# Performance work log

Hardware: AMD Instinct MI355X
Metric: run time of the kernel (lower is better)

The kernel has to match this reference:

```python
import jax, jax.numpy as jnp
import numpy as np
import math

def setup_inputs() -> dict:
    key = jax.random.key(0)
    k1, k2, k3 = jax.random.split(key, 3)
    B, S, E = 2, 2048, 1024
    H, D = 16, 64
    inputs = jax.random.normal(k1, (B, S, E), dtype=jnp.float32)
    Wqkv = jax.random.uniform(k2, (E, 3 * H * D), minval=-0.1, maxval=0.1, dtype=jnp.float32)
    Wo = jax.random.uniform(k3, (H * D, E), minval=-0.1, maxval=0.1, dtype=jnp.float32)
    return {"inputs": inputs, "Wqkv": Wqkv, "Wo": Wo, "nhead": H}

def reference(inputs, Wqkv, Wo, nhead):
    B, S, E = inputs.shape
    H = int(nhead)
    D = Wqkv.shape[1] // (3 * H)
    causal, ghost = True, True

    qkv = jnp.matmul(inputs, Wqkv)                       # (B, S, 3*H*D)
    qkv = qkv.reshape(B, S, 3, H, D)
    Q = qkv[:, :, 0].transpose(0, 2, 1, 3)               # (B, H, S, D)
    K = qkv[:, :, 1].transpose(0, 2, 1, 3)
    V = qkv[:, :, 2].transpose(0, 2, 1, 3)

    scores = jnp.einsum('bhqd,bhkd->bhqk', Q, K) / math.sqrt(D)
    if causal:
        neg_inf = jnp.float32(-jnp.inf)
        mask = jnp.where(jnp.triu(jnp.ones((S, S), dtype=bool), k=1), neg_inf, jnp.float32(0.0))
        scores = scores + mask  # broadcast over (B, H)

    # ghost softmax: standard stable softmax but denominator gets +1
    z = jnp.exp(scores - jnp.max(scores, axis=-1, keepdims=True))
    denom = jnp.sum(z, axis=-1, keepdims=True)
    if ghost:
        denom = denom + jnp.float32(1.0)
    attn = z / denom                                      # (B, H, S, S)

    A = jnp.einsum('bhqk,bhkd->bhqd', attn, V)            # (B, H, S, D)
    A = A.transpose(0, 2, 1, 3).reshape(B, S, H * D)      # (B, S, H*D)
    return jnp.matmul(A, Wo)
```

## Files before the change

kernel.cpp:

```cpp
#include <hip/hip_runtime.h>

typedef float    f32x4  __attribute__((ext_vector_type(4)));
typedef _Float16 half8  __attribute__((ext_vector_type(8)));
typedef _Float16 half4v __attribute__((ext_vector_type(4)));

#define MFMA16(a,b,c) __builtin_amdgcn_mfma_f32_16x16x32_f16(a,b,c,0,0,0)

__device__ __forceinline__ float exp2_fast(float x){
  float y; asm("v_exp_f32 %0, %1" : "=v"(y) : "v"(x)); return y;
}
__device__ __forceinline__ void gload_lds16(const _Float16* g, _Float16* l){
  __builtin_amdgcn_global_load_lds(
      (const __attribute__((address_space(1))) unsigned int*)(g),
      (__attribute__((address_space(3))) unsigned int*)(l),
      16, 0, 0);
}

#define S_LEN 2048
#define E_DIM 1024
#define H_NUM 16
#define D_DIM 64
#define NBH   32
#define M_ROWS 4096
#define N3    3072
#define LOG2E 1.44269504089f

__global__ __launch_bounds__(256) void prep_kernel(
    const float* __restrict__ X, const float* __restrict__ Wqkv,
    const float* __restrict__ Wo,
    _Float16* __restrict__ Xh, _Float16* __restrict__ Wqh,
    _Float16* __restrict__ Woh)
{
  __shared__ float tile[32][33];
  const int blk = blockIdx.x, tid = threadIdx.x;
  if (blk < 4096){
    const int i = blk * 256 + tid;
    const float4 v = reinterpret_cast<const float4*>(X)[i];
    half4v h;
    h[0] = (_Float16)v.x; h[1] = (_Float16)v.y;
    h[2] = (_Float16)v.z; h[3] = (_Float16)v.w;
    *reinterpret_cast<half4v*>(&Xh[(size_t)i*4]) = h;
    return;
  }
  const float* in; _Float16* out; int R, C, bx, by;
  if (blk < 4096 + 3072){
    const int b2 = blk - 4096;
    in = Wqkv; out = Wqh; R = E_DIM; C = N3;
    bx = (b2 % 96) * 32; by = (b2 / 96) * 32;
  } else {
    const int b2 = blk - 7168;
    in = Wo; out = Woh; R = E_DIM; C = E_DIM;
    bx = (b2 % 32) * 32; by = (b2 / 32) * 32;
  }
  const int tx = tid & 31, ty = tid >> 5;
#pragma unroll
  for (int i = ty; i < 32; i += 8)
    tile[i][tx] = in[(size_t)(by + i) * C + bx + tx];
  __syncthreads();
#pragma unroll
  for (int i = ty; i < 32; i += 8)
    out[(size_t)(bx + i) * R + by + tx] = (_Float16)tile[tx][i];
}

template<int EPI>
__global__ __launch_bounds__(256, 3) void gemm97(
    const _Float16* __restrict__ A, const _Float16* __restrict__ B,
    int Kdim, int Ndim, float* __restrict__ Cout,
    _Float16* __restrict__ qh, _Float16* __restrict__ kh, _Float16* __restrict__ vh)
{
  __shared__ __align__(16) _Float16 sA[128][64], sB[128][64];
  const int tid = threadIdx.x;
  const int nx = gridDim.x, nwg = nx * gridDim.y;
  int bidx = blockIdx.x, bidy = blockIdx.y;
  if ((nwg & 7) == 0){
    const int id = bidx + nx * bidy;
    const int nid = (id & 7) * (nwg >> 3) + (id >> 3);
    bidx = nid % nx; bidy = nid / nx;
  }
  const int m0 = bidy * 128, n0 = bidx * 128;
  const int wid = tid >> 6, lane = tid & 63;
  const int wr = (wid >> 1) * 64, wc = (wid & 1) * 64;
  const int lr = lane & 15, lc = lane >> 4;
  const int ldrow = lane >> 3;
  const int ldcol = ((lane & 7) ^ ldrow) * 8;
  const int swz = (lr & 7) << 4;

  f32x4 acc[4][4] = {};
  const int nK = Kdim >> 6;
  for (int ks = 0; ks < nK; ++ks){
    const int k0 = ks << 6;
#pragma unroll
    for (int cc = 0; cc < 4; ++cc){
      const int c = wid * 4 + cc;
      const int row = c * 8 + ldrow;
      gload_lds16(&A[(size_t)(m0 + row) * Kdim + k0 + ldcol], &sA[c*8][0]);
      gload_lds16(&B[(size_t)(n0 + row) * Kdim + k0 + ldcol], &sB[c*8][0]);
    }
    __syncthreads();
    const char* ab = (const char*)&sA[0][0];
    const char* bb = (const char*)&sB[0][0];
#pragma unroll
    for (int kk = 0; kk < 64; kk += 32){
      half8 fa[4], fb[4];
#pragma unroll
      for (int t = 0; t < 4; ++t){
        fa[t] = *reinterpret_cast<const half8*>(
            ab + (wr + t*16 + lr)*128 + ((kk*2 + lc*16) ^ swz));
        fb[t] = *reinterpret_cast<const half8*>(
            bb + (wc + t*16 + lr)*128 + ((kk*2 + lc*16) ^ swz));
      }
#pragma unroll
      for (int mt = 0; mt < 4; ++mt)
#pragma unroll
        for (int nt = 0; nt < 4; ++nt)
          acc[mt][nt] = MFMA16(fa[mt], fb[nt], acc[mt][nt]);
    }
    __syncthreads();
  }
#pragma unroll
  for (int mt = 0; mt < 4; ++mt)
#pragma unroll
    for (int nt = 0; nt < 4; ++nt)
#pragma unroll
      for (int r = 0; r < 4; ++r){
        const int m = m0 + wr + mt*16 + lc*4 + r;
        const int n = n0 + wc + nt*16 + lr;
        float v = acc[mt][nt][r];
        if (EPI == 0){
          Cout[(size_t)m * Ndim + n] = v;
        } else {
          const int t = n >> 10, rem = n & 1023, hh = rem >> 6, d = rem & 63;
          const int b = m >> 11, s = m & 2047;
          const int bh = b * H_NUM + hh;
          if (t == 0) v *= (0.125f * LOG2E);
          size_t o;
          if (t == 2)  o = ((size_t)bh * D_DIM + d) * S_LEN + s;
          else         o = ((size_t)bh * S_LEN + s) * D_DIM + d;
          _Float16* ph = (t == 0) ? qh : (t == 1) ? kh : vh;
          ph[o] = (_Float16)v;
        }
      }
}

__global__ __launch_bounds__(256, 4) void gemm64(
    const _Float16* __restrict__ A, const _Float16* __restrict__ B,
    int Kdim, int Ndim, float* __restrict__ Cout)
{
  __shared__ __align__(16) _Float16 sA[64][64], sB[128][64];
  const int tid = threadIdx.x;
  const int nx = gridDim.x, nwg = nx * gridDim.y;
  int bidx = blockIdx.x, bidy = blockIdx.y;
  if ((nwg & 7) == 0){
    const int id = bidx + nx * bidy;
    const int nid = (id & 7) * (nwg >> 3) + (id >> 3);
    bidx = nid % nx; bidy = nid / nx;
  }
  const int m0 = bidy * 64, n0 = bidx * 128;
  const int wid = tid >> 6, lane = tid & 63;
  const int wr = (wid >> 1) * 32, wc = (wid & 1) * 64;
  const int lr = lane & 15, lc = lane >> 4;
  const int ldrow = lane >> 3;
  const int ldcol = ((lane & 7) ^ ldrow) * 8;
  const int swz = (lr & 7) << 4;

  f32x4 acc[2][4] = {};
  const int nK = Kdim >> 6;
  for (int ks = 0; ks < nK; ++ks){
    const int k0 = ks << 6;
#pragma unroll
    for (int cc = 0; cc < 2; ++cc){
      const int c = wid * 2 + cc;
      const int row = c * 8 + ldrow;
      gload_lds16(&A[(size_t)(m0 + row) * Kdim + k0 + ldcol], &sA[c*8][0]);
    }
#pragma unroll
    for (int cc = 0; cc < 4; ++cc){
      const int c = wid * 4 + cc;
      const int row = c * 8 + ldrow;
      gload_lds16(&B[(size_t)(n0 + row) * Kdim + k0 + ldcol], &sB[c*8][0]);
    }
    __syncthreads();
    const char* ab = (const char*)&sA[0][0];
    const char* bb = (const char*)&sB[0][0];
#pragma unroll
    for (int kk = 0; kk < 64; kk += 32){
      half8 fa[2], fb[4];
#pragma unroll
      for (int t = 0; t < 2; ++t)
        fa[t] = *reinterpret_cast<const half8*>(
            ab + (wr + t*16 + lr)*128 + ((kk*2 + lc*16) ^ swz));
#pragma unroll
      for (int t = 0; t < 4; ++t)
        fb[t] = *reinterpret_cast<const half8*>(
            bb + (wc + t*16 + lr)*128 + ((kk*2 + lc*16) ^ swz));
#pragma unroll
      for (int mt = 0; mt < 2; ++mt)
#pragma unroll
        for (int nt = 0; nt < 4; ++nt)
          acc[mt][nt] = MFMA16(fa[mt], fb[nt], acc[mt][nt]);
    }
    __syncthreads();
  }
#pragma unroll
  for (int mt = 0; mt < 2; ++mt)
#pragma unroll
    for (int nt = 0; nt < 4; ++nt)
#pragma unroll
      for (int r = 0; r < 4; ++r){
        const int m = m0 + wr + mt*16 + lc*4 + r;
        const int n = n0 + wc + nt*16 + lr;
        Cout[(size_t)m * Ndim + n] = acc[mt][nt][r];
      }
}

__global__ __launch_bounds__(256, 6) void attn_partial(
    const _Float16* __restrict__ Qh, const _Float16* __restrict__ Kh,
    const _Float16* __restrict__ Vth,
    _Float16* __restrict__ Opart, float* __restrict__ Spart)
{
  __shared__ __align__(16) _Float16 sK[64][64];
  __shared__ __align__(16) _Float16 sV[64][64];
  __shared__ __align__(16) _Float16 sP[4][16][64];
  const int tid = threadIdx.x, wid = tid >> 6, lane = tid & 63;
  const int id  = blockIdx.x;
  const int xcd = id & 7, seq = id >> 3;
  const int bh  = xcd + 8 * (seq & 3);
  const int rest = seq >> 2;
  const int qt  = 31 - (rest >> 1);
  const int half = rest & 1;
  const int h0 = (qt + 1) >> 1;
  const int t0 = half ? h0 : 0;
  const int t1 = half ? (qt + 1) : h0;
  const int q0 = qt * 64;
  const int lr = lane & 15, lc = lane >> 4;
  const int swz = (lr & 7) << 4;
  const size_t base = (size_t)bh * S_LEN * D_DIM;

  const int pidx = (bh * 32 + qt) * 2 + half;
  _Float16* Op = Opart + (size_t)pidx * 4096;
  float*    Sp = Spart + (size_t)pidx * 192;

  if (t1 <= t0){
#pragma unroll
    for (int dt = 0; dt < 4; ++dt)
#pragma unroll
      for (int r = 0; r < 4; ++r)
        Op[(wid*16 + lc*4 + r)*64 + dt*16 + lr] = (_Float16)0.f;
    if (lane < 16){
      Sp[wid*16 + lr] = -1e30f;
      Sp[64 + wid*16 + lr] = 0.f;
      Sp[128 + wid*16 + lr] = -1e30f;
    }
    return;
  }

  const int lrow = lane >> 3;
  const int cswz = ((lane & 7) ^ lrow) * 8;

  auto stage = [&](int t){
    const int kv0 = t * 64;
#pragma unroll
    for (int cc = 0; cc < 2; ++cc){
      const int ch = wid * 2 + cc;
      const int row = ch * 8 + lrow;
      gload_lds16(&Kh[base + (size_t)(kv0 + row) * D_DIM + cswz], &sK[ch*8][0]);
      gload_lds16(&Vth[base + (size_t)row * S_LEN + kv0 + cswz], &sV[ch*8][0]);
    }
  };

  half8 fq[2];
  {
    const int qrow = q0 + wid*16 + lr;
#pragma unroll
    for (int kc = 0; kc < 2; ++kc)
      fq[kc] = *reinterpret_cast<const half8*>(&Qh[base + (size_t)qrow * 64 + kc*32 + lc*8]);
  }

  f32x4 acc[4] = {};
  float m = -1e30f, l = 0.f, tm = -1e30f;

#pragma unroll 1
  for (int t = t0; t < t1; ++t){
    __syncthreads();
    stage(t);
    __syncthreads();

    const char* kb = (const char*)&sK[0][0];
    f32x4 sc[4];
    __builtin_amdgcn_s_setprio(1);
#pragma unroll
    for (int nt = 0; nt < 4; ++nt){
      f32x4 z = {};
#pragma unroll
      for (int kc = 0; kc < 2; ++kc){
        const half8 fk = *reinterpret_cast<const half8*>(
            kb + (nt*16 + lr)*128 + ((kc*64 + lc*16) ^ swz));
        z = MFMA16(fk, fq[kc], z);
      }
      sc[nt] = z;
    }
    __builtin_amdgcn_s_setprio(0);

    if (t == qt){
#pragma unroll
      for (int nt = 0; nt < 4; ++nt)
#pragma unroll
        for (int r = 0; r < 4; ++r)
          if (nt*16 + lc*4 + r > wid*16 + lr) sc[nt][r] = -1e30f;
    }

    f32x4 a;
#pragma unroll
    for (int j = 0; j < 4; ++j)
      a[j] = fmaxf(fmaxf(sc[0][j], sc[1][j]), fmaxf(sc[2][j], sc[3][j]));
    float mx = fmaxf(fmaxf(a[0], a[1]), fmaxf(a[2], a[3]));
    mx = fmaxf(mx, __shfl_xor(mx, 16));
    mx = fmaxf(mx, __shfl_xor(mx, 32));
    tm = fmaxf(tm, mx);

    if (__any(mx > m + 8.0f)){
      const float mn = fmaxf(m, mx);
      const float s = exp2_fast(m - mn);
      l *= s; m = mn;
      float rs[4];
#pragma unroll
      for (int r = 0; r < 4; ++r)
        rs[r] = __shfl(s, (lc << 4) | (lc*4 + r), 64);
#pragma unroll
      for (int dt = 0; dt < 4; ++dt)
#pragma unroll
        for (int r = 0; r < 4; ++r) acc[dt][r] *= rs[r];
    }

    f32x4 ssum = {};
#pragma unroll
    for (int nt = 0; nt < 4; ++nt){
#pragma unroll
      for (int r = 0; r < 4; ++r) sc[nt][r] = exp2_fast(sc[nt][r] - m);
      ssum += sc[nt];
    }
    float s1 = (ssum[0] + ssum[1]) + (ssum[2] + ssum[3]);
    s1 += __shfl_xor(s1, 16);
    s1 += __shfl_xor(s1, 32);
    l += s1;

    char* pw = (char*)&sP[wid][0][0];
#pragma unroll
    for (int nt = 0; nt < 4; ++nt){
      int2 pk;
      pk.x = __builtin_bit_cast(int, __builtin_amdgcn_cvt_pkrtz(sc[nt][0], sc[nt][1]));
      pk.y = __builtin_bit_cast(int, __builtin_amdgcn_cvt_pkrtz(sc[nt][2], sc[nt][3]));
      *reinterpret_cast<int2*>(pw + lr*128 + ((nt*32 + lc*8) ^ swz)) = pk;
    }

    const half8 pa0 = *reinterpret_cast<const half8*>(pw + lr*128 + ((lc*16) ^ swz));
    const half8 pa1 = *reinterpret_cast<const half8*>(pw + lr*128 + ((64 + lc*16) ^ swz));

    const char* vb = (const char*)&sV[0][0];
    __builtin_amdgcn_s_setprio(1);
#pragma unroll
    for (int dt = 0; dt < 4; ++dt){
#pragma unroll
      for (int kc = 0; kc < 2; ++kc){
        const half8 fv = *reinterpret_cast<const half8*>(
            vb + (dt*16 + lr)*128 + ((kc*64 + lc*16) ^ swz));
        acc[dt] = MFMA16(kc ? pa1 : pa0, fv, acc[dt]);
      }
    }
    __builtin_amdgcn_s_setprio(0);
  }

#pragma unroll
  for (int dt = 0; dt < 4; ++dt)
#pragma unroll
    for (int r = 0; r < 4; ++r)
      Op[(wid*16 + lc*4 + r)*64 + dt*16 + lr] = (_Float16)acc[dt][r];
  if (lane < 16){
    Sp[wid*16 + lr] = m;
    Sp[64 + wid*16 + lr] = l;
    Sp[128 + wid*16 + lr] = tm;
  }
}

__global__ __launch_bounds__(256) void attn_merge(
    const _Float16* __restrict__ Opart, const float* __restrict__ Spart,
    _Float16* __restrict__ Ao)
{
  const int id = blockIdx.x;
  const int bh = id >> 5, qt = id & 31;
  const int tid = threadIdx.x;
  const int row = tid >> 2, seg = tid & 3;
  const int p0 = (bh * 32 + qt) * 2, p1 = p0 + 1;
  const float* S1 = Spart + (size_t)p0 * 192;
  const float* S2 = Spart + (size_t)p1 * 192;
  const float m1 = S1[row], l1 = S1[64 + row], t1 = S1[128 + row];
  const float m2 = S2[row], l2 = S2[64 + row], t2 = S2[128 + row];
  const float M  = fmaxf(m1, m2);
  const float w1 = exp2_fast(m1 - M), w2 = exp2_fast(m2 - M);
  const float den = l1 * w1 + l2 * w2 + exp2_fast(fmaxf(t1, t2) - M);
  const float inv = 1.0f / den;
  const half8* O1 = reinterpret_cast<const half8*>(Opart + (size_t)p0 * 4096 + row * 64 + seg * 16);
  const half8* O2 = reinterpret_cast<const half8*>(Opart + (size_t)p1 * 4096 + row * 64 + seg * 16);
  const int b = bh >> 4, hh = bh & 15;
  const int q = qt * 64 + row;
  _Float16* dst = Ao + ((size_t)(b * S_LEN + q)) * E_DIM + hh * D_DIM + seg * 16;
#pragma unroll
  for (int v = 0; v < 2; ++v){
    const half8 a1 = O1[v], a2 = O2[v];
    half8 o;
#pragma unroll
    for (int j = 0; j < 8; ++j)
      o[j] = (_Float16)(((float)a1[j] * w1 + (float)a2[j] * w2) * inv);
    reinterpret_cast<half8*>(dst)[v] = o;
  }
}

extern "C" void kernel_launch(void* const* d_in, const int* in_sizes, int n_in,
                              void* d_out, int out_size, void* d_ws, size_t ws_size,
                              hipStream_t stream){
  const float* X    = (const float*)d_in[0];
  const float* Wqkv = (const float*)d_in[1];
  const float* Wo   = (const float*)d_in[2];
  float* out = (float*)d_out;

  _Float16* w = (_Float16*)d_ws;
  size_t off = 0;
  auto alloc = [&](size_t n){ _Float16* p = w + off; off += n; return p; };
  const size_t ME   = (size_t)M_ROWS * E_DIM;
  const size_t WQ   = (size_t)N3 * E_DIM;
  const size_t WOsz = (size_t)E_DIM * E_DIM;
  const size_t QK   = (size_t)NBH * S_LEN * D_DIM;
  _Float16 *Xh = alloc(ME);
  _Float16 *Wqh = alloc(WQ);
  _Float16 *Woh = alloc(WOsz);
  _Float16 *Qh = alloc(QK), *Kh = alloc(QK), *Vth = alloc(QK);
  _Float16 *Ahalf = alloc(ME);
  _Float16 *Opart = alloc((size_t)2048 * 4096);
  _Float16 *Sraw  = alloc((size_t)2048 * 192 * 2);
  float* Spart = (float*)Sraw;

  prep_kernel<<<dim3(8192), 256, 0, stream>>>(X, Wqkv, Wo, Xh, Wqh, Woh);

  gemm97<1><<<dim3(N3/128, M_ROWS/128), 256, 0, stream>>>(
      Xh, Wqh, E_DIM, N3, nullptr, Qh, Kh, Vth);

  attn_partial<<<dim3(2048), 256, 0, stream>>>(Qh, Kh, Vth, Opart, Spart);
  attn_merge<<<dim3(1024), 256, 0, stream>>>(Opart, Spart, Ahalf);

  gemm64<<<dim3(E_DIM/128, M_ROWS/64), 256, 0, stream>>>(
      Ahalf, Woh, E_DIM, E_DIM, out);
}
```

Baseline: 111.3 us.

## Fuse attention partial merge into output projection GEMM prologue

Drops the separate attn_merge kernel and the intermediate fp16 attention buffer. The output-projection GEMM now computes the per-row merge weights into a shared-memory table, then builds each A tile by loading both partial outputs, blending them in registers and storing the result to LDS with the same swizzle as before. This removes one launch plus a full write and read of the merged activations. In exchange, each of the 8 column blocks redoes the merge with double partial reads (likely mostly L2 hits), the A tile loses its async global-to-LDS path, and launch bounds fall to 2 waves per EU.

```diff
diff --git a/kernel.cpp b/kernel.cpp
--- a/kernel.cpp
+++ b/kernel.cpp
@@ -142,11 +142,12 @@
       }
 }
 
-__global__ __launch_bounds__(256, 4) void gemm64(
-    const _Float16* __restrict__ A, const _Float16* __restrict__ B,
-    int Kdim, int Ndim, float* __restrict__ Cout)
+__global__ __launch_bounds__(256, 2) void gemm64f(
+    const _Float16* __restrict__ Opart, const float* __restrict__ Spart,
+    const _Float16* __restrict__ B, float* __restrict__ Cout)
 {
   __shared__ __align__(16) _Float16 sA[64][64], sB[128][64];
+  __shared__ float wTab[16][64][2];
   const int tid = threadIdx.x;
   const int nx = gridDim.x, nwg = nx * gridDim.y;
   int bidx = blockIdx.x, bidy = blockIdx.y;
@@ -156,6 +157,8 @@
     bidx = nid % nx; bidy = nid / nx;
   }
   const int m0 = bidy * 64, n0 = bidx * 128;
+  const int b  = m0 >> 11;
+  const int qt = (m0 & 2047) >> 6;
   const int wid = tid >> 6, lane = tid & 63;
   const int wr = (wid >> 1) * 32, wc = (wid & 1) * 64;
   const int lr = lane & 15, lc = lane >> 4;
@@ -163,21 +166,45 @@
   const int ldcol = ((lane & 7) ^ ldrow) * 8;
   const int swz = (lr & 7) << 4;
 
+  for (int j = tid; j < 1024; j += 256){
+    const int hh = j >> 6, row = j & 63;
+    const int pb = ((b * H_NUM + hh) * 32 + qt) * 2;
+    const float* S1 = Spart + (size_t)pb * 192;
+    const float* S2 = S1 + 192;
+    const float m1 = S1[row], l1 = S1[64 + row], t1v = S1[128 + row];
+    const float m2 = S2[row], l2 = S2[64 + row], t2v = S2[128 + row];
+    const float M  = fmaxf(m1, m2);
+    const float w1 = exp2_fast(m1 - M), w2 = exp2_fast(m2 - M);
+    const float den = l1 * w1 + l2 * w2 + exp2_fast(fmaxf(t1v, t2v) - M);
+    const float inv = 1.0f / den;
+    wTab[hh][row][0] = w1 * inv;
+    wTab[hh][row][1] = w2 * inv;
+  }
+  __syncthreads();
+
   f32x4 acc[2][4] = {};
-  const int nK = Kdim >> 6;
-  for (int ks = 0; ks < nK; ++ks){
+  for (int ks = 0; ks < 16; ++ks){
     const int k0 = ks << 6;
+    const int pbase = ((b * H_NUM + ks) * 32 + qt) * 2;
+    const _Float16* O1 = Opart + (size_t)pbase * 4096;
+    const _Float16* O2 = O1 + 4096;
 #pragma unroll
     for (int cc = 0; cc < 2; ++cc){
-      const int c = wid * 2 + cc;
-      const int row = c * 8 + ldrow;
-      gload_lds16(&A[(size_t)(m0 + row) * Kdim + k0 + ldcol], &sA[c*8][0]);
+      const int row = (wid * 2 + cc) * 8 + ldrow;
+      const half8 a1 = *reinterpret_cast<const half8*>(&O1[row * 64 + ldcol]);
+      const half8 a2 = *reinterpret_cast<const half8*>(&O2[row * 64 + ldcol]);
+      const float w1 = wTab[ks][row][0], w2 = wTab[ks][row][1];
+      half8 av;
+#pragma unroll
+      for (int j = 0; j < 8; ++j)
+        av[j] = (_Float16)((float)a1[j] * w1 + (float)a2[j] * w2);
+      *reinterpret_cast<half8*>((char*)&sA[0][0] + row * 128 + (lane & 7) * 16) = av;
     }
 #pragma unroll
     for (int cc = 0; cc < 4; ++cc){
       const int c = wid * 4 + cc;
       const int row = c * 8 + ldrow;
-      gload_lds16(&B[(size_t)(n0 + row) * Kdim + k0 + ldcol], &sB[c*8][0]);
+      gload_lds16(&B[(size_t)(n0 + row) * E_DIM + k0 + ldcol], &sB[c*8][0]);
     }
     __syncthreads();
     const char* ab = (const char*)&sA[0][0];
@@ -209,7 +236,7 @@
       for (int r = 0; r < 4; ++r){
         const int m = m0 + wr + mt*16 + lc*4 + r;
         const int n = n0 + wc + nt*16 + lr;
-        Cout[(size_t)m * Ndim + n] = acc[mt][nt][r];
+        Cout[(size_t)m * E_DIM + n] = acc[mt][nt][r];
       }
 }
 
@@ -382,39 +409,6 @@
   }
 }
 
-__global__ __launch_bounds__(256) void attn_merge(
-    const _Float16* __restrict__ Opart, const float* __restrict__ Spart,
-    _Float16* __restrict__ Ao)
-{
-  const int id = blockIdx.x;
-  const int bh = id >> 5, qt = id & 31;
-  const int tid = threadIdx.x;
-  const int row = tid >> 2, seg = tid & 3;
-  const int p0 = (bh * 32 + qt) * 2, p1 = p0 + 1;
-  const float* S1 = Spart + (size_t)p0 * 192;
-  const float* S2 = Spart + (size_t)p1 * 192;
-  const float m1 = S1[row], l1 = S1[64 + row], t1 = S1[128 + row];
-  const float m2 = S2[row], l2 = S2[64 + row], t2 = S2[128 + row];
-  const float M  = fmaxf(m1, m2);
-  const float w1 = exp2_fast(m1 - M), w2 = exp2_fast(m2 - M);
-  const float den = l1 * w1 + l2 * w2 + exp2_fast(fmaxf(t1, t2) - M);
-  const float inv = 1.0f / den;
-  const half8* O1 = reinterpret_cast<const half8*>(Opart + (size_t)p0 * 4096 + row * 64 + seg * 16);
-  const half8* O2 = reinterpret_cast<const half8*>(Opart + (size_t)p1 * 4096 + row * 64 + seg * 16);
-  const int b = bh >> 4, hh = bh & 15;
-  const int q = qt * 64 + row;
-  _Float16* dst = Ao + ((size_t)(b * S_LEN + q)) * E_DIM + hh * D_DIM + seg * 16;
-#pragma unroll
-  for (int v = 0; v < 2; ++v){
-    const half8 a1 = O1[v], a2 = O2[v];
-    half8 o;
-#pragma unroll
-    for (int j = 0; j < 8; ++j)
-      o[j] = (_Float16)(((float)a1[j] * w1 + (float)a2[j] * w2) * inv);
-    reinterpret_cast<half8*>(dst)[v] = o;
-  }
-}
-
 extern "C" void kernel_launch(void* const* d_in, const int* in_sizes, int n_in,
                               void* d_out, int out_size, void* d_ws, size_t ws_size,
                               hipStream_t stream){
@@ -434,7 +428,6 @@
   _Float16 *Wqh = alloc(WQ);
   _Float16 *Woh = alloc(WOsz);
   _Float16 *Qh = alloc(QK), *Kh = alloc(QK), *Vth = alloc(QK);
-  _Float16 *Ahalf = alloc(ME);
   _Float16 *Opart = alloc((size_t)2048 * 4096);
   _Float16 *Sraw  = alloc((size_t)2048 * 192 * 2);
   float* Spart = (float*)Sraw;
@@ -445,8 +438,7 @@
       Xh, Wqh, E_DIM, N3, nullptr, Qh, Kh, Vth);
 
   attn_partial<<<dim3(2048), 256, 0, stream>>>(Qh, Kh, Vth, Opart, Spart);
-  attn_merge<<<dim3(1024), 256, 0, stream>>>(Opart, Spart, Ahalf);
-
-  gemm64<<<dim3(E_DIM/128, M_ROWS/64), 256, 0, stream>>>(
-      Ahalf, Woh, E_DIM, E_DIM, out);
-}
+
+  gemm64f<<<dim3(E_DIM/128, M_ROWS/64), 256, 0, stream>>>(
+      Opart, Spart, Woh, out);
+}
```

New measurement: 112.9 us. No clear change (+1.5%).
